# Optimization experiments

Hardware: AMD Instinct MI355X
Metric: run time of the kernel (lower is better)

## Reference

```python
import jax, jax.numpy as jnp
import numpy as np

B, N, KD, VD, ID, H = 2, 2048, 1024, 1024, 1024, 16
HD = ID // H
SCALE = ID ** (-0.5)  # module quirk: scale uses inner_dim, not head_dim
EPS = 1e-5


def layernorm(x, g, b):
    mu = jnp.mean(x, axis=-1, keepdims=True)
    var = jnp.var(x, axis=-1, keepdims=True)
    return (x - mu) * jax.lax.rsqrt(var + EPS) * g + b


def setup_inputs() -> dict:
    key = jax.random.key(0)
    ks = jax.random.split(key, 12)
    d = {
        "keys": jax.random.normal(ks[0], (B, N, KD), jnp.float32),
        "values": jax.random.normal(ks[1], (B, N, VD), jnp.float32),
        "qk_norm_g": jnp.ones((KD,), jnp.float32),
        "qk_norm_b": jnp.zeros((KD,), jnp.float32),
        "value_norm_g": jnp.ones((VD,), jnp.float32),
        "value_norm_b": jnp.zeros((VD,), jnp.float32),
        "key_norm_g": jnp.ones((ID,), jnp.float32),
        "key_norm_b": jnp.zeros((ID,), jnp.float32),
        "query_norm_g": jnp.ones((ID,), jnp.float32),
        "query_norm_b": jnp.zeros((ID,), jnp.float32),
        "w_qk": jax.random.normal(ks[2], (KD, 2 * ID), jnp.float32) * (KD ** -0.5),
        "w_v": jax.random.normal(ks[3], (VD, ID), jnp.float32) * (VD ** -0.5),
        "w_out": jax.random.normal(ks[4], (ID, VD), jnp.float32) * (ID ** -0.5),
        "b_out": jnp.zeros((VD,), jnp.float32),
    }
    return d


def reference(keys, values, qk_norm_g, qk_norm_b, value_norm_g, value_norm_b,
              key_norm_g, key_norm_b, query_norm_g, query_norm_b,
              w_qk, w_v, w_out, b_out):
    keys = layernorm(keys, qk_norm_g, qk_norm_b)
    values = layernorm(values, value_norm_g, value_norm_b)
    qk = keys @ w_qk  # [B,N,2*ID]
    q, k = qk[..., :ID], qk[..., ID:]
    q = layernorm(q, query_norm_g, query_norm_b)
    k = layernorm(k, key_norm_g, key_norm_b)
    # b n (h d) -> b h n d
    q = q.reshape(B, N, H, HD).transpose(0, 2, 1, 3)
    k = k.reshape(B, N, H, HD).transpose(0, 2, 1, 3)
    v = (values @ w_v).reshape(B, N, H, HD).transpose(0, 2, 1, 3)
    dots = jnp.einsum('bhqd,bhkd->bhqk', q, k) * SCALE
    attn = jax.nn.softmax(dots, axis=-1)
    out = jnp.einsum('bhqk,bhkd->bhqd', attn, v)
    out = out.transpose(0, 2, 1, 3).reshape(B, N, ID)
    return out @ w_out + b_out
```

## Files before the change

### kernel.cpp

```cpp
#include <hip/hip_runtime.h>
#include <hip/hip_bf16.h>
#include <type_traits>


typedef __hip_bfloat16 bf16;
typedef __attribute__((ext_vector_type(8))) short bf16x8;
typedef __attribute__((ext_vector_type(4))) float f32x4;

#define MFMA_BF16(a, b, c) __builtin_amdgcn_mfma_f32_16x16x32_bf16((a), (b), (c), 0, 0, 0)

__device__ __forceinline__ float us2f(unsigned short u) {
  unsigned int v = ((unsigned int)u) << 16;
  return __builtin_bit_cast(float, v);
}

__device__ __forceinline__ unsigned pack_bf16x2(float a, float b) {
  union { __hip_bfloat162 h; unsigned u; } cv;
  cv.h = __float22bfloat162_rn(float2{a, b});
  return cv.u;
}

__device__ __forceinline__ unsigned pack_bf16x2_trunc(float a, float b) {
  return __builtin_amdgcn_perm(__builtin_bit_cast(unsigned, b),
                               __builtin_bit_cast(unsigned, a), 0x07060302u);
}

__device__ __forceinline__ void gl_lds16(const bf16* g, bf16* l) {
  __builtin_amdgcn_global_load_lds(
      (const __attribute__((address_space(1))) void*)g,
      (__attribute__((address_space(3))) void*)l, 16, 0, 0);
}

template <typename TIN>
__global__ __launch_bounds__(256) void ln2_kernel(
    const TIN* __restrict__ in0, const TIN* __restrict__ in1, int stride,
    const float* __restrict__ g0, const float* __restrict__ b0,
    const float* __restrict__ g1, const float* __restrict__ b1,
    bf16* __restrict__ out0, bf16* __restrict__ out1, int D,
    float sc0, float sc1)
{
  const int which = blockIdx.y;
  const TIN* in = which ? in1 : in0;
  const float* gamma = which ? g1 : g0;
  const float* beta = which ? b1 : b0;
  bf16* out = which ? out1 : out0;
  const float sc = which ? sc1 : sc0;
  const int row = blockIdx.x;
  const int t = threadIdx.x;
  float x0, x1, x2, x3;
  if constexpr (std::is_same_v<TIN, float>) {
    float4 u = *(const float4*)(in + (size_t)row * stride + t * 4);
    x0 = u.x; x1 = u.y; x2 = u.z; x3 = u.w;
  } else {
    ushort4 u = *(const ushort4*)(in + (size_t)row * stride + t * 4);
    x0 = us2f(u.x); x1 = us2f(u.y); x2 = us2f(u.z); x3 = us2f(u.w);
  }
  float s = x0 + x1 + x2 + x3;
  float s2 = x0 * x0 + x1 * x1 + x2 * x2 + x3 * x3;
#pragma unroll
  for (int m = 1; m < 64; m <<= 1) {
    s += __shfl_xor(s, m);
    s2 += __shfl_xor(s2, m);
  }
  __shared__ float red[10];
  const int w = t >> 6, lane = t & 63;
  if (lane == 0) { red[w] = s; red[4 + w] = s2; }
  __syncthreads();
  if (t == 0) {
    float S = red[0] + red[1] + red[2] + red[3];
    float S2 = red[4] + red[5] + red[6] + red[7];
    float mu = S / (float)D;
    float var = S2 / (float)D - mu * mu;
    red[8] = mu;
    red[9] = rsqrtf(var + 1e-5f);
  }
  __syncthreads();
  const float mu = red[8], rs = red[9];
  float4 g4 = *(const float4*)(gamma + t * 4);
  float4 b4 = *(const float4*)(beta + t * 4);
  uint2 o;
  o.x = pack_bf16x2(((x0 - mu) * rs * g4.x + b4.x) * sc, ((x1 - mu) * rs * g4.y + b4.y) * sc);
  o.y = pack_bf16x2(((x2 - mu) * rs * g4.z + b4.z) * sc, ((x3 - mu) * rs * g4.w + b4.w) * sc);
  *(uint2*)(out + (size_t)row * D + t * 4) = o;
}

__global__ __launch_bounds__(256) void transpose3_kernel(
    const float* __restrict__ s0, bf16* __restrict__ d0,
    const float* __restrict__ s1, bf16* __restrict__ d1,
    const float* __restrict__ s2, bf16* __restrict__ d2)
{
  const int z = blockIdx.z;
  if (z > 0 && blockIdx.x >= 16) return;
  const float* in = (z == 0) ? s0 : (z == 1) ? s1 : s2;
  bf16* out = (z == 0) ? d0 : (z == 1) ? d1 : d2;
  const int R = 1024, C = (z == 0) ? 2048 : 1024;
  __shared__ float tile[64][68];
  const int r0 = blockIdx.y * 64, c0 = blockIdx.x * 64;
  const int t = threadIdx.x;
  const int lr = t >> 2, lc = (t & 3) * 16;
  const float* src = in + (size_t)(r0 + lr) * C + (c0 + lc);
#pragma unroll
  for (int i = 0; i < 4; ++i) {
    float4 u = *(const float4*)(src + i * 4);
    tile[lr][lc + i * 4 + 0] = u.x;
    tile[lr][lc + i * 4 + 1] = u.y;
    tile[lr][lc + i * 4 + 2] = u.z;
    tile[lr][lc + i * 4 + 3] = u.w;
  }
  __syncthreads();
  __align__(16) bf16 tmp[16];
#pragma unroll
  for (int j = 0; j < 16; ++j) tmp[j] = __float2bfloat16(tile[lc + j][lr]);
  bf16* dst = out + (size_t)(c0 + lr) * R + (r0 + lc);
  *(bf16x8*)dst       = *(const bf16x8*)&tmp[0];
  *(bf16x8*)(dst + 8) = *(const bf16x8*)&tmp[8];
}

template <int BM, int BN, int TMODE, typename TOUT>
__global__ __launch_bounds__(256) void gemm_bt_kernel(
    const bf16* __restrict__ A, const bf16* __restrict__ Bt,
    const float* __restrict__ bias, TOUT* __restrict__ C,
    int M, int N, int K, int has_bias)
{
  constexpr int MT = BM / 32, NT = BN / 32;
  constexpr int ASL = BM / 32, BSL = BN / 32;
  __shared__ __align__(16) bf16 lA[BM * 64];
  __shared__ __align__(16) bf16 lB[BN * 64];
  constexpr int OUTSZ = (TMODE == 1) ? 128 * 68 : 1;
  __shared__ __align__(16) bf16 lOut[OUTSZ];
  const int t = threadIdx.x;
  const int w = t >> 6, lane = t & 63, l15 = lane & 15, quad = lane >> 4;
  const int wy = w >> 1, wx = w & 1;
  const bf16* Ab = A + (size_t)blockIdx.y * BM * K;
  const bf16* Bb = Bt + (size_t)blockIdx.x * BN * K;
  f32x4 acc[MT][NT] = {};

  const int sw = (quad ^ (l15 & 7)) << 3;

  for (int kc = 0; kc < K; kc += 64) {
    __syncthreads();
#pragma unroll
    for (int i = 0; i < ASL; ++i) {
      int s = i * 256 + t;
      int row = s >> 3, c = (s & 7) ^ (row & 7);
      gl_lds16(Ab + (size_t)row * K + kc + (c << 3), lA + s * 8);
    }
#pragma unroll
    for (int i = 0; i < BSL; ++i) {
      int s = i * 256 + t;
      int row = s >> 3, c = (s & 7) ^ (row & 7);
      gl_lds16(Bb + (size_t)row * K + kc + (c << 3), lB + s * 8);
    }
    __syncthreads();

    bf16x8 af[MT][2], bfr[NT][2];
#pragma unroll
    for (int mt = 0; mt < MT; ++mt) {
      const int r = wy * (BM / 2) + mt * 16 + l15;
      af[mt][0] = *(const bf16x8*)&lA[r * 64 + sw];
      af[mt][1] = *(const bf16x8*)&lA[r * 64 + (sw ^ 32)];
    }
#pragma unroll
    for (int nt = 0; nt < NT; ++nt) {
      const int r = wx * (BN / 2) + nt * 16 + l15;
      bfr[nt][0] = *(const bf16x8*)&lB[r * 64 + sw];
      bfr[nt][1] = *(const bf16x8*)&lB[r * 64 + (sw ^ 32)];
    }
#pragma unroll
    for (int mt = 0; mt < MT; ++mt)
#pragma unroll
      for (int nt = 0; nt < NT; ++nt) {
        acc[mt][nt] = MFMA_BF16(af[mt][0], bfr[nt][0], acc[mt][nt]);
        acc[mt][nt] = MFMA_BF16(af[mt][1], bfr[nt][1], acc[mt][nt]);
      }
  }

  if constexpr (TMODE == 1) {
    __syncthreads();
#pragma unroll
    for (int mt = 0; mt < MT; ++mt)
#pragma unroll
      for (int nt = 0; nt < NT; ++nt) {
        const int d = wx * (BN / 2) + nt * 16 + l15;
        const int n = wy * 32 + mt * 16 + quad * 4;
        uint2 pk;
        pk.x = pack_bf16x2(acc[mt][nt][0], acc[mt][nt][1]);
        pk.y = pack_bf16x2(acc[mt][nt][2], acc[mt][nt][3]);
        *(uint2*)&lOut[d * 68 + n] = pk;
      }
    __syncthreads();
    const int row0 = blockIdx.y * BM;
    const int bidx = row0 >> 11, n0 = row0 & 2047;
    const int col0 = blockIdx.x * BN;
    const int d = t >> 1, half = (t & 1) * 32;
    const bf16* srcp = &lOut[d * 68 + half];
    __align__(16) bf16 tmp[32];
#pragma unroll
    for (int j = 0; j < 8; ++j)
      *(uint2*)&tmp[j * 4] = *(const uint2*)(srcp + j * 4);
    bf16* g = (bf16*)C + ((size_t)(bidx << 10) + col0 + d) * 2048 + n0 + half;
#pragma unroll
    for (int j = 0; j < 4; ++j)
      *(bf16x8*)(g + j * 8) = *(const bf16x8*)&tmp[j * 8];
  } else {
    const int row_base = blockIdx.y * BM + wy * (BM / 2);
    const int col_base = blockIdx.x * BN + wx * (BN / 2);
#pragma unroll
    for (int mt = 0; mt < MT; ++mt)
#pragma unroll
      for (int nt = 0; nt < NT; ++nt) {
        const int col = col_base + nt * 16 + l15;
        const float bb = has_bias ? bias[col] : 0.0f;
#pragma unroll
        for (int r = 0; r < 4; ++r) {
          const int row = row_base + mt * 16 + quad * 4 + r;
          float v = acc[mt][nt][r] + bb;
          if constexpr (std::is_same_v<TOUT, bf16>)
            C[(size_t)row * N + col] = __float2bfloat16(v);
          else
            C[(size_t)row * N + col] = v;
        }
      }
  }
}

__global__ __launch_bounds__(256) void flash_kernel(
    const bf16* __restrict__ Q, const bf16* __restrict__ Km,
    const bf16* __restrict__ Vt, bf16* __restrict__ O)
{
  __shared__ __align__(16) bf16 smem[9216 + 8192 + 8192 + 8192];
  bf16* lP = smem;
  bf16* lQ = smem + 9216;
  bf16* lKb = smem + 9216 + 8192;
  bf16* lVb = smem + 9216 + 8192 + 8192;
  const int t = threadIdx.x;
  const int w = t >> 6, lane = t & 63, l15 = lane & 15, quad = lane >> 4;
  const int qt = blockIdx.x, bh = blockIdx.y;
  const int b = bh >> 4, h = bh & 15;
  const int qrow0 = b * 2048 + qt * 128;
  const bf16* qbase = Q + (size_t)qrow0 * 1024 + h * 64;
  const bf16* kbase = Km + ((size_t)(b * 2048)) * 1024 + h * 64;
  const bf16* vbase = Vt + ((size_t)(b * 1024 + h * 64)) * 2048;
  bf16* lPm = lP + w * (32 * 72);

  const int sr0 = t >> 3, sc0 = ((t & 7) ^ (sr0 & 7)) << 3;
  const int sr1 = (256 + t) >> 3, sc1 = (((256 + t) & 7) ^ (sr1 & 7)) << 3;
  const bf16* kp0 = kbase + sr0 * 1024 + sc0;
  const bf16* kp1 = kbase + sr1 * 1024 + sc1;
  const bf16* vp0 = vbase + sr0 * 2048 + sc0;
  const bf16* vp1 = vbase + sr1 * 2048 + sc1;

#pragma unroll
  for (int i = 0; i < 4; ++i) {
    int s = i * 256 + t;
    int row = s >> 3, c = (s & 7) ^ (row & 7);
    gl_lds16(qbase + (size_t)row * 1024 + (c << 3), lQ + s * 8);
  }
  gl_lds16(kp0, lKb + t * 8);
  gl_lds16(kp1, lKb + (256 + t) * 8);
  gl_lds16(vp0, lVb + t * 8);
  gl_lds16(vp1, lVb + (256 + t) * 8);
  asm volatile("s_waitcnt vmcnt(4)" ::: "memory");
  __builtin_amdgcn_s_barrier();

  const int sw = (quad ^ (l15 & 7)) << 3;
  bf16x8 qf[2][2];
#pragma unroll
  for (int mset = 0; mset < 2; ++mset) {
    const int row = w * 32 + mset * 16 + l15;
    qf[mset][0] = *(const bf16x8*)&lQ[row * 64 + sw];
    qf[mset][1] = *(const bf16x8*)&lQ[row * 64 + (sw ^ 32)];
  }

  f32x4 o_acc[4][2] = {};
  f32x4 l_vec[2] = {};

  for (int kt = 0; kt < 32; ++kt) {
    const int cur = kt & 1;
    bf16* lK = lKb + cur * 4096;
    bf16* lV = lVb + cur * 4096;
    bf16* lKn = lKb + (cur ^ 1) * 4096;
    bf16* lVn = lVb + (cur ^ 1) * 4096;

    __builtin_amdgcn_s_barrier();
    {
      const int ktn = (kt + 1) & 31;
      const int ko = ktn << 16;
      const int vo = ktn << 6;
      gl_lds16(kp0 + ko, lKn + t * 8);
      gl_lds16(kp1 + ko, lKn + (256 + t) * 8);
      gl_lds16(vp0 + vo, lVn + t * 8);
      gl_lds16(vp1 + vo, lVn + (256 + t) * 8);
    }
    asm volatile("s_waitcnt vmcnt(4)" ::: "memory");
    __builtin_amdgcn_s_barrier();

    bf16x8 kf[4][2];
#pragma unroll
    for (int nt = 0; nt < 4; ++nt) {
      kf[nt][0] = *(const bf16x8*)&lK[(nt * 16 + l15) * 64 + sw];
      kf[nt][1] = *(const bf16x8*)&lK[(nt * 16 + l15) * 64 + (sw ^ 32)];
    }

#pragma unroll
    for (int mset = 0; mset < 2; ++mset) {
#pragma unroll
      for (int nt = 0; nt < 4; ++nt) {
        f32x4 z = {};
        z = MFMA_BF16(kf[nt][0], qf[mset][0], z);
        z = MFMA_BF16(kf[nt][1], qf[mset][1], z);
        f32x4 p;
#pragma unroll
        for (int r = 0; r < 4; ++r) p[r] = __builtin_amdgcn_exp2f(z[r]);
        l_vec[mset] += p;
        uint2 pk;
        pk.x = pack_bf16x2_trunc(p[0], p[1]);
        pk.y = pack_bf16x2_trunc(p[2], p[3]);
        *(uint2*)&lPm[(mset * 16 + l15) * 72 + nt * 16 + quad * 4] = pk;
      }
    }

    bf16x8 vf[4][2];
#pragma unroll
    for (int dt = 0; dt < 4; ++dt) {
      vf[dt][0] = *(const bf16x8*)&lV[(dt * 16 + l15) * 64 + sw];
      vf[dt][1] = *(const bf16x8*)&lV[(dt * 16 + l15) * 64 + (sw ^ 32)];
    }
    asm volatile("s_waitcnt lgkmcnt(0)" ::: "memory");

#pragma unroll
    for (int mset = 0; mset < 2; ++mset) {
      const bf16* pr = &lPm[(mset * 16 + l15) * 72 + quad * 8];
      bf16x8 pf0 = *(const bf16x8*)pr;
      bf16x8 pf1 = *(const bf16x8*)(pr + 32);
#pragma unroll
      for (int dt = 0; dt < 4; ++dt) {
        o_acc[dt][mset] = MFMA_BF16(vf[dt][0], pf0, o_acc[dt][mset]);
        o_acc[dt][mset] = MFMA_BF16(vf[dt][1], pf1, o_acc[dt][mset]);
      }
    }
  }

#pragma unroll
  for (int mset = 0; mset < 2; ++mset) {
    float tsum = l_vec[mset][0] + l_vec[mset][1] + l_vec[mset][2] + l_vec[mset][3];
    tsum += __shfl_xor(tsum, 16);
    tsum += __shfl_xor(tsum, 32);
    const float inv = 1.0f / tsum;
    const int m = qrow0 + w * 32 + mset * 16 + l15;
#pragma unroll
    for (int dt = 0; dt < 4; ++dt) {
      uint2 ok;
      ok.x = pack_bf16x2(o_acc[dt][mset][0] * inv, o_acc[dt][mset][1] * inv);
      ok.y = pack_bf16x2(o_acc[dt][mset][2] * inv, o_acc[dt][mset][3] * inv);
      *(uint2*)&O[(size_t)m * 1024 + h * 64 + dt * 16 + quad * 4] = ok;
    }
  }
}

extern "C" void kernel_launch(void* const* d_in, const int* in_sizes, int n_in,
                              void* d_out, int out_size, void* d_ws, size_t ws_size,
                              hipStream_t stream)
{
  (void)in_sizes; (void)n_in; (void)out_size; (void)ws_size;
  const float* keys   = (const float*)d_in[0];
  const float* values = (const float*)d_in[1];
  const float* qk_g   = (const float*)d_in[2];
  const float* qk_b   = (const float*)d_in[3];
  const float* val_g  = (const float*)d_in[4];
  const float* val_b  = (const float*)d_in[5];
  const float* key_g  = (const float*)d_in[6];
  const float* key_b  = (const float*)d_in[7];
  const float* qry_g  = (const float*)d_in[8];
  const float* qry_b  = (const float*)d_in[9];
  const float* w_qk   = (const float*)d_in[10];
  const float* w_v    = (const float*)d_in[11];
  const float* w_out  = (const float*)d_in[12];
  const float* b_out  = (const float*)d_in[13];
  float* out = (float*)d_out;

  const float CEXP = 0.03125f * 1.44269504f;

  char* ws = (char*)d_ws;
  const size_t MB = 1024 * 1024;
  bf16* keys_ln   = (bf16*)(ws + 0);
  bf16* values_ln = (bf16*)(ws + 8 * MB);
  bf16* qk        = (bf16*)(ws + 16 * MB);
  bf16* attn      = (bf16*)(ws + 16 * MB);
  bf16* vt        = (bf16*)(ws + 24 * MB);
  bf16* qln       = (bf16*)(ws + 32 * MB);
  bf16* kln       = (bf16*)(ws + 40 * MB);
  bf16* wqkT      = (bf16*)(ws + 48 * MB);
  bf16* wvT       = (bf16*)(ws + 52 * MB);
  bf16* woutT     = (bf16*)(ws + 54 * MB);

  ln2_kernel<float><<<dim3(4096, 2), 256, 0, stream>>>(
      keys, values, 1024, qk_g, qk_b, val_g, val_b, keys_ln, values_ln, 1024, 1.0f, 1.0f);
  transpose3_kernel<<<dim3(32, 16, 3), 256, 0, stream>>>(w_qk, wqkT, w_v, wvT, w_out, woutT);
  gemm_bt_kernel<64, 128, 0, bf16><<<dim3(16, 64), 256, 0, stream>>>(keys_ln, wqkT, nullptr, qk, 4096, 2048, 1024, 0);
  ln2_kernel<bf16><<<dim3(4096, 2), 256, 0, stream>>>(
      qk, qk + 1024, 2048, qry_g, qry_b, key_g, key_b, qln, kln, 1024, CEXP, 1.0f);
  gemm_bt_kernel<64, 128, 1, bf16><<<dim3(8, 64), 256, 0, stream>>>(values_ln, wvT, nullptr, vt, 4096, 1024, 1024, 0);
  flash_kernel<<<dim3(16, 32), 256, 0, stream>>>(qln, kln, vt, attn);
  gemm_bt_kernel<64, 128, 0, float><<<dim3(8, 64), 256, 0, stream>>>(attn, woutT, b_out, out, 4096, 1024, 1024, 1);
}
```

Measured before the change: 245.8 us.

## Double-buffer GEMM LDS staging and enlarge tiles to 128x128

Rewrites the GEMM main loop to double-buffer the A/B tiles in shared memory, prefetching the next K chunk while MFMAs run on the current one, with explicit vmcnt waits and raw barriers. Global pointers are precomputed once, and fragment loads are split into two halves to lower register pressure. All three GEMMs move from 64x128 to 128x128 tiles, which halves the grid and doubles per-block reuse. The transposed-output epilogue reuses the staging buffer and writes straight from LDS. The costs are more LDS per block and fewer blocks, which may reduce occupancy and load balance.

```diff
diff --git a/kernel.cpp b/kernel.cpp
--- a/kernel.cpp
+++ b/kernel.cpp
@@ -124,10 +124,8 @@
 {
   constexpr int MT = BM / 32, NT = BN / 32;
   constexpr int ASL = BM / 32, BSL = BN / 32;
-  __shared__ __align__(16) bf16 lA[BM * 64];
-  __shared__ __align__(16) bf16 lB[BN * 64];
-  constexpr int OUTSZ = (TMODE == 1) ? 128 * 68 : 1;
-  __shared__ __align__(16) bf16 lOut[OUTSZ];
+  constexpr int BUFE = (BM + BN) * 64;
+  __shared__ __align__(16) bf16 smem[2 * BUFE];
   const int t = threadIdx.x;
   const int w = t >> 6, lane = t & 63, l15 = lane & 15, quad = lane >> 4;
   const int wy = w >> 1, wx = w & 1;
@@ -135,73 +133,89 @@
   const bf16* Bb = Bt + (size_t)blockIdx.x * BN * K;
   f32x4 acc[MT][NT] = {};
 
+  const bf16* aptr[ASL];
+  const bf16* bptr[BSL];
+#pragma unroll
+  for (int i = 0; i < ASL; ++i) {
+    int s = i * 256 + t, row = s >> 3, c = (s & 7) ^ (row & 7);
+    aptr[i] = Ab + (size_t)row * K + (c << 3);
+  }
+#pragma unroll
+  for (int i = 0; i < BSL; ++i) {
+    int s = i * 256 + t, row = s >> 3, c = (s & 7) ^ (row & 7);
+    bptr[i] = Bb + (size_t)row * K + (c << 3);
+  }
+
+  auto stage = [&](bf16* buf, int kc) {
+#pragma unroll
+    for (int i = 0; i < ASL; ++i)
+      gl_lds16(aptr[i] + kc, buf + (i * 256 + t) * 8);
+#pragma unroll
+    for (int i = 0; i < BSL; ++i)
+      gl_lds16(bptr[i] + kc, buf + BM * 64 + (i * 256 + t) * 8);
+  };
+
   const int sw = (quad ^ (l15 & 7)) << 3;
-
-  for (int kc = 0; kc < K; kc += 64) {
-    __syncthreads();
-#pragma unroll
-    for (int i = 0; i < ASL; ++i) {
-      int s = i * 256 + t;
-      int row = s >> 3, c = (s & 7) ^ (row & 7);
-      gl_lds16(Ab + (size_t)row * K + kc + (c << 3), lA + s * 8);
-    }
-#pragma unroll
-    for (int i = 0; i < BSL; ++i) {
-      int s = i * 256 + t;
-      int row = s >> 3, c = (s & 7) ^ (row & 7);
-      gl_lds16(Bb + (size_t)row * K + kc + (c << 3), lB + s * 8);
-    }
-    __syncthreads();
-
-    bf16x8 af[MT][2], bfr[NT][2];
-#pragma unroll
-    for (int mt = 0; mt < MT; ++mt) {
-      const int r = wy * (BM / 2) + mt * 16 + l15;
-      af[mt][0] = *(const bf16x8*)&lA[r * 64 + sw];
-      af[mt][1] = *(const bf16x8*)&lA[r * 64 + (sw ^ 32)];
-    }
-#pragma unroll
-    for (int nt = 0; nt < NT; ++nt) {
-      const int r = wx * (BN / 2) + nt * 16 + l15;
-      bfr[nt][0] = *(const bf16x8*)&lB[r * 64 + sw];
-      bfr[nt][1] = *(const bf16x8*)&lB[r * 64 + (sw ^ 32)];
-    }
-#pragma unroll
-    for (int mt = 0; mt < MT; ++mt)
-#pragma unroll
-      for (int nt = 0; nt < NT; ++nt) {
-        acc[mt][nt] = MFMA_BF16(af[mt][0], bfr[nt][0], acc[mt][nt]);
-        acc[mt][nt] = MFMA_BF16(af[mt][1], bfr[nt][1], acc[mt][nt]);
-      }
+  const int NK = K >> 6;
+
+  stage(smem, 0);
+
+  for (int kt = 0; kt < NK; ++kt) {
+    const int cur = kt & 1;
+    bf16* lA = smem + cur * BUFE;
+    bf16* lB = lA + BM * 64;
+    __builtin_amdgcn_s_barrier();
+    if (kt + 1 < NK) {
+      stage(smem + (cur ^ 1) * BUFE, (kt + 1) << 6);
+      asm volatile("s_waitcnt vmcnt(8)" ::: "memory");
+    } else {
+      asm volatile("s_waitcnt vmcnt(0)" ::: "memory");
+    }
+    __builtin_amdgcn_s_barrier();
+
+#pragma unroll
+    for (int h = 0; h < 2; ++h) {
+      const int so = sw ^ (h << 5);
+      bf16x8 af[MT], bfr[NT];
+#pragma unroll
+      for (int mt = 0; mt < MT; ++mt)
+        af[mt] = *(const bf16x8*)&lA[(wy * (BM / 2) + mt * 16 + l15) * 64 + so];
+#pragma unroll
+      for (int nt = 0; nt < NT; ++nt)
+        bfr[nt] = *(const bf16x8*)&lB[(wx * (BN / 2) + nt * 16 + l15) * 64 + so];
+#pragma unroll
+      for (int mt = 0; mt < MT; ++mt)
+#pragma unroll
+        for (int nt = 0; nt < NT; ++nt)
+          acc[mt][nt] = MFMA_BF16(af[mt], bfr[nt], acc[mt][nt]);
+    }
   }
 
   if constexpr (TMODE == 1) {
+    constexpr int STR = BM + 8;
+    bf16* lOut = smem;
     __syncthreads();
 #pragma unroll
     for (int mt = 0; mt < MT; ++mt)
 #pragma unroll
       for (int nt = 0; nt < NT; ++nt) {
         const int d = wx * (BN / 2) + nt * 16 + l15;
-        const int n = wy * 32 + mt * 16 + quad * 4;
+        const int n = wy * (BM / 2) + mt * 16 + quad * 4;
         uint2 pk;
         pk.x = pack_bf16x2(acc[mt][nt][0], acc[mt][nt][1]);
         pk.y = pack_bf16x2(acc[mt][nt][2], acc[mt][nt][3]);
-        *(uint2*)&lOut[d * 68 + n] = pk;
+        *(uint2*)&lOut[d * STR + n] = pk;
       }
     __syncthreads();
     const int row0 = blockIdx.y * BM;
     const int bidx = row0 >> 11, n0 = row0 & 2047;
     const int col0 = blockIdx.x * BN;
-    const int d = t >> 1, half = (t & 1) * 32;
-    const bf16* srcp = &lOut[d * 68 + half];
-    __align__(16) bf16 tmp[32];
-#pragma unroll
-    for (int j = 0; j < 8; ++j)
-      *(uint2*)&tmp[j * 4] = *(const uint2*)(srcp + j * 4);
+    const int d = t >> 1, half = (t & 1) * (BM / 2);
+    const bf16* srcp = &lOut[d * STR + half];
     bf16* g = (bf16*)C + ((size_t)(bidx << 10) + col0 + d) * 2048 + n0 + half;
 #pragma unroll
-    for (int j = 0; j < 4; ++j)
-      *(bf16x8*)(g + j * 8) = *(const bf16x8*)&tmp[j * 8];
+    for (int j = 0; j < BM / 16; ++j)
+      *(bf16x8*)(g + j * 8) = *(const bf16x8*)(srcp + j * 8);
   } else {
     const int row_base = blockIdx.y * BM + wy * (BM / 2);
     const int col_base = blockIdx.x * BN + wx * (BN / 2);
@@ -397,10 +411,10 @@
   ln2_kernel<float><<<dim3(4096, 2), 256, 0, stream>>>(
       keys, values, 1024, qk_g, qk_b, val_g, val_b, keys_ln, values_ln, 1024, 1.0f, 1.0f);
   transpose3_kernel<<<dim3(32, 16, 3), 256, 0, stream>>>(w_qk, wqkT, w_v, wvT, w_out, woutT);
-  gemm_bt_kernel<64, 128, 0, bf16><<<dim3(16, 64), 256, 0, stream>>>(keys_ln, wqkT, nullptr, qk, 4096, 2048, 1024, 0);
+  gemm_bt_kernel<128, 128, 0, bf16><<<dim3(16, 32), 256, 0, stream>>>(keys_ln, wqkT, nullptr, qk, 4096, 2048, 1024, 0);
   ln2_kernel<bf16><<<dim3(4096, 2), 256, 0, stream>>>(
       qk, qk + 1024, 2048, qry_g, qry_b, key_g, key_b, qln, kln, 1024, CEXP, 1.0f);
-  gemm_bt_kernel<64, 128, 1, bf16><<<dim3(8, 64), 256, 0, stream>>>(values_ln, wvT, nullptr, vt, 4096, 1024, 1024, 0);
+  gemm_bt_kernel<128, 128, 1, bf16><<<dim3(8, 32), 256, 0, stream>>>(values_ln, wvT, nullptr, vt, 4096, 1024, 1024, 0);
   flash_kernel<<<dim3(16, 32), 256, 0, stream>>>(qln, kln, vt, attn);
-  gemm_bt_kernel<64, 128, 0, float><<<dim3(8, 64), 256, 0, stream>>>(attn, woutT, b_out, out, 4096, 1024, 1024, 1);
-}
+  gemm_bt_kernel<128, 128, 0, float><<<dim3(8, 32), 256, 0, stream>>>(attn, woutT, b_out, out, 4096, 1024, 1024, 1);
+}
```

Result: faster. 240.7 us (-2.1%).
